# Kernel optimization log

Measured on AMD Instinct MI355X. Metric: run time of the kernel, lower is better.

## Reference

```python
import jax, jax.numpy as jnp
import numpy as np

N, T, D, H = 256, 128, 512, 1024

def setup_inputs() -> dict:
    key = jax.random.key(0)
    k = jax.random.split(key, 5)
    x = jax.random.normal(k[0], (N, T, D), dtype=jnp.float32)
    A = jax.random.normal(k[1], (N, H, 4, 4), dtype=jnp.float32)
    Wx = jax.random.normal(k[2], (D, 4 * H), dtype=jnp.float32) / np.sqrt(D)
    Wh = jax.random.normal(k[3], (H, 4 * H), dtype=jnp.float32) / np.sqrt(H)
    Wattn = jax.random.normal(k[4], (H, 4 * H), dtype=jnp.float32) / np.sqrt(H)
    b = jnp.zeros((4 * H,), dtype=jnp.float32)
    return {"x": x, "A": A, "Wx": Wx, "Wh": Wh, "Wattn": Wattn, "b": b}

def reference(x, A, Wx, Wh, Wattn, b):
    n, h_dim = A.shape[0], A.shape[1]
    A_flat = A.reshape(n, h_dim, -1)            # (N, H, L), L = 16 spatial locations
    h0 = A_flat.mean(axis=-1)                   # avg-pooled image feature
    c0 = h0
    scale = 1.0 / jnp.sqrt(jnp.asarray(h_dim, dtype=x.dtype))

    def step(carry, x_t):
        h, c = carry
        # scaled dot-product attention over the 4x4 feature grid
        scores = jnp.einsum('nhl,nh->nl', A_flat, h) * scale
        w = jax.nn.softmax(scores, axis=1)
        attn = jnp.einsum('nhl,nl->nh', A_flat, w)
        gates = x_t @ Wx + h @ Wh + attn @ Wattn + b  # (N, 4H)
        i, f, o, g = jnp.split(gates, 4, axis=1)
        c_next = jax.nn.sigmoid(f) * c + jax.nn.sigmoid(i) * jnp.tanh(g)
        h_next = jax.nn.sigmoid(o) * jnp.tanh(c_next)
        return (h_next, c_next), h_next

    (_, _), hs = jax.lax.scan(step, (h0, c0), jnp.swapaxes(x, 0, 1))
    return jnp.swapaxes(hs, 0, 1)               # (N, T, H)
```

## Files before the change

### kernel.cpp

```cpp
#include <hip/hip_runtime.h>

#define Nn 256
#define Tt 128
#define Dd 512
#define Hh 1024
#define G4 4096
#define KK 2560
#define KHALF 1280

typedef __attribute__((ext_vector_type(8))) short s8v;
typedef __attribute__((ext_vector_type(4))) float f4v;

__device__ __forceinline__ float bf2f(ushort u) {
    union { unsigned int i; float f; } v; v.i = ((unsigned int)u) << 16; return v.f;
}
__device__ __forceinline__ ushort f2bf(float f) {
    union { float f; unsigned int i; } v; v.f = f;
    unsigned int x = v.i;
    return (ushort)((x + 0x7fffu + ((x >> 16) & 1u)) >> 16);
}
__device__ __forceinline__ void split2(float f, ushort& hi, ushort& lo) {
    hi = f2bf(f);
    lo = f2bf(f - bf2f(hi));
}

__global__ __launch_bounds__(256) void prep_W(
    const float* __restrict__ Wx, const float* __restrict__ Wh,
    const float* __restrict__ Wa, ushort* __restrict__ Whi,
    ushort* __restrict__ Wlo)
{
    __shared__ float tile[64 * 65];
    int kb = blockIdx.x * 64;
    int jb = blockIdx.y * 64;
    const float* src; int kofs;
    if (kb < Dd)            { src = Wx; kofs = kb; }
    else if (kb < Dd + Hh)  { src = Wh; kofs = kb - Dd; }
    else                    { src = Wa; kofs = kb - Dd - Hh; }
    int tid = threadIdx.x;
    int r = tid >> 2;
    int c16 = (tid & 3) * 16;
    const float* sp = src + (size_t)(kofs + r) * G4 + jb + c16;
    #pragma unroll
    for (int i = 0; i < 16; i++) tile[(c16 + i) * 65 + r] = sp[i];
    __syncthreads();
    ushort hi[16], lo[16];
    #pragma unroll
    for (int i = 0; i < 16; i++) split2(tile[r * 65 + c16 + i], hi[i], lo[i]);
    size_t o = (size_t)(jb + r) * KK + kb + c16;
    #pragma unroll
    for (int p = 0; p < 2; p++) {
        s8v vh, vl;
        #pragma unroll
        for (int i = 0; i < 8; i++) { vh[i] = (short)hi[p * 8 + i]; vl[i] = (short)lo[p * 8 + i]; }
        *(s8v*)&Whi[o + p * 8] = vh;
        *(s8v*)&Wlo[o + p * 8] = vl;
    }
}

__global__ __launch_bounds__(256) void init_h0(
    const float* __restrict__ A, float* __restrict__ h, float* __restrict__ c,
    ushort* __restrict__ hhi, ushort* __restrict__ hlo)
{
    int i = blockIdx.x * 256 + threadIdx.x;
    const float* ap = A + (size_t)i * 16;
    float s = 0.f;
    #pragma unroll
    for (int l = 0; l < 16; l++) s += ap[l];
    s *= (1.f / 16.f);
    h[i] = s; c[i] = s;
    ushort hi, lo; split2(s, hi, lo);
    hhi[i] = hi; hlo[i] = lo;
}

__global__ __launch_bounds__(256) void attn_step(
    const float* __restrict__ A, const float* __restrict__ h,
    ushort* __restrict__ athi, ushort* __restrict__ atlo)
{
    int n = blockIdx.x;
    int tid = threadIdx.x;
    int lane = tid & 63, wave = tid >> 6;
    __shared__ float red[4][16];
    __shared__ float wsm[16];
    const float* An = A + (size_t)n * Hh * 16;
    float areg[4][16];
    float hreg[4];
    #pragma unroll
    for (int rr = 0; rr < 4; rr++) {
        int hh = tid + rr * 256;
        const f4v* ap = (const f4v*)(An + (size_t)hh * 16);
        #pragma unroll
        for (int q = 0; q < 4; q++) {
            f4v v = ap[q];
            areg[rr][q * 4 + 0] = v[0]; areg[rr][q * 4 + 1] = v[1];
            areg[rr][q * 4 + 2] = v[2]; areg[rr][q * 4 + 3] = v[3];
        }
        hreg[rr] = h[n * Hh + hh];
    }
    float part[16];
    #pragma unroll
    for (int l = 0; l < 16; l++) part[l] = 0.f;
    #pragma unroll
    for (int rr = 0; rr < 4; rr++)
        #pragma unroll
        for (int l = 0; l < 16; l++) part[l] += areg[rr][l] * hreg[rr];
    #pragma unroll
    for (int l = 0; l < 16; l++) {
        float v = part[l];
        #pragma unroll
        for (int off = 32; off > 0; off >>= 1) v += __shfl_down(v, off);
        if (lane == 0) red[wave][l] = v;
    }
    __syncthreads();
    if (tid == 0) {
        float sc[16]; float mx = -3.4e38f;
        #pragma unroll
        for (int l = 0; l < 16; l++) {
            sc[l] = (red[0][l] + red[1][l] + red[2][l] + red[3][l]) * 0.03125f;
            mx = fmaxf(mx, sc[l]);
        }
        float sum = 0.f;
        #pragma unroll
        for (int l = 0; l < 16; l++) { sc[l] = expf(sc[l] - mx); sum += sc[l]; }
        float inv = 1.f / sum;
        #pragma unroll
        for (int l = 0; l < 16; l++) wsm[l] = sc[l] * inv;
    }
    __syncthreads();
    float w[16];
    #pragma unroll
    for (int l = 0; l < 16; l++) w[l] = wsm[l];
    #pragma unroll
    for (int rr = 0; rr < 4; rr++) {
        int hh = tid + rr * 256;
        float s = 0.f;
        #pragma unroll
        for (int l = 0; l < 16; l++) s += areg[rr][l] * w[l];
        ushort hi, lo; split2(s, hi, lo);
        athi[n * Hh + hh] = hi; atlo[n * Hh + hh] = lo;
    }
}

__global__ __launch_bounds__(256) void gemm_half(
    const float* __restrict__ x,
    const ushort* __restrict__ hhi, const ushort* __restrict__ hlo,
    const ushort* __restrict__ athi, const ushort* __restrict__ atlo,
    const ushort* __restrict__ Whi, const ushort* __restrict__ Wlo,
    float* __restrict__ g0, float* __restrict__ g1, int t)
{
    __shared__ ushort Ahi[64 * 72], Alo[64 * 72];
    __shared__ ushort Bhi[64 * 72], Blo[64 * 72];
    int j0 = blockIdx.x * 64;
    int n0 = blockIdx.y * 64;
    int kb0 = blockIdx.z * KHALF;
    float* gout = blockIdx.z ? g1 : g0;
    int tid = threadIdx.x;
    int lane = tid & 63, wave = tid >> 6;
    int l15 = lane & 15, quad = lane >> 4;
    f4v acc[4];
    #pragma unroll
    for (int s = 0; s < 4; s++) acc[s] = (f4v){0.f, 0.f, 0.f, 0.f};

    int rs = tid >> 3;
    int cs = (tid & 7) * 8;

    for (int kb = kb0; kb < kb0 + KHALF; kb += 64) {
        __syncthreads();
        if (kb < Dd) {
            const float* xs = x + (size_t)t * Dd + kb + cs;
            #pragma unroll
            for (int p = 0; p < 2; p++) {
                int r = rs + 32 * p;
                const float* ap = xs + (size_t)(n0 + r) * (Tt * Dd);
                s8v vh, vl;
                #pragma unroll
                for (int i = 0; i < 8; i++) {
                    ushort hi_, lo_; split2(ap[i], hi_, lo_);
                    vh[i] = (short)hi_; vl[i] = (short)lo_;
                }
                *(s8v*)&Ahi[r * 72 + cs] = vh;
                *(s8v*)&Alo[r * 72 + cs] = vl;
            }
        } else {
            const ushort *sh, *sl; int kofs;
            if (kb < Dd + Hh) { sh = hhi; sl = hlo; kofs = kb - Dd; }
            else              { sh = athi; sl = atlo; kofs = kb - Dd - Hh; }
            #pragma unroll
            for (int p = 0; p < 2; p++) {
                int r = rs + 32 * p;
                size_t o = (size_t)(n0 + r) * Hh + kofs + cs;
                *(s8v*)&Ahi[r * 72 + cs] = *(const s8v*)&sh[o];
                *(s8v*)&Alo[r * 72 + cs] = *(const s8v*)&sl[o];
            }
        }
        #pragma unroll
        for (int p = 0; p < 2; p++) {
            int r = rs + 32 * p;
            size_t o = (size_t)(j0 + r) * KK + kb + cs;
            *(s8v*)&Bhi[r * 72 + cs] = *(const s8v*)&Whi[o];
            *(s8v*)&Blo[r * 72 + cs] = *(const s8v*)&Wlo[o];
        }
        __syncthreads();
        #pragma unroll
        for (int ks = 0; ks < 2; ks++) {
            s8v ah = *(const s8v*)&Ahi[(wave * 16 + l15) * 72 + ks * 32 + quad * 8];
            s8v al = *(const s8v*)&Alo[(wave * 16 + l15) * 72 + ks * 32 + quad * 8];
            #pragma unroll
            for (int s = 0; s < 4; s++) {
                s8v bh = *(const s8v*)&Bhi[(s * 16 + l15) * 72 + ks * 32 + quad * 8];
                s8v bl = *(const s8v*)&Blo[(s * 16 + l15) * 72 + ks * 32 + quad * 8];
                acc[s] = __builtin_amdgcn_mfma_f32_16x16x32_bf16(ah, bh, acc[s], 0, 0, 0);
                acc[s] = __builtin_amdgcn_mfma_f32_16x16x32_bf16(ah, bl, acc[s], 0, 0, 0);
                acc[s] = __builtin_amdgcn_mfma_f32_16x16x32_bf16(al, bh, acc[s], 0, 0, 0);
            }
        }
    }
    #pragma unroll
    for (int s = 0; s < 4; s++) {
        int j = j0 + s * 16 + l15;
        #pragma unroll
        for (int rr = 0; rr < 4; rr++) {
            int row = n0 + wave * 16 + quad * 4 + rr;
            gout[(size_t)row * G4 + j] = acc[s][rr];
        }
    }
}

__global__ __launch_bounds__(256) void lstm_update(
    const float* __restrict__ g0, const float* __restrict__ g1,
    const float* __restrict__ bias,
    float* __restrict__ c, float* __restrict__ h,
    ushort* __restrict__ hhi, ushort* __restrict__ hlo,
    float* __restrict__ out, int t)
{
    int i = blockIdx.x * 256 + threadIdx.x;
    int n = i >> 10, j = i & 1023;
    size_t base = (size_t)n * G4;
    float gi = g0[base + j]          + g1[base + j]          + bias[j];
    float gf = g0[base + Hh + j]     + g1[base + Hh + j]     + bias[Hh + j];
    float go = g0[base + 2 * Hh + j] + g1[base + 2 * Hh + j] + bias[2 * Hh + j];
    float gg = g0[base + 3 * Hh + j] + g1[base + 3 * Hh + j] + bias[3 * Hh + j];
    float si = 1.f / (1.f + expf(-gi));
    float sf = 1.f / (1.f + expf(-gf));
    float so = 1.f / (1.f + expf(-go));
    float tg = tanhf(gg);
    float cn = sf * c[i] + si * tg;
    float hn = so * tanhf(cn);
    c[i] = cn; h[i] = hn;
    ushort hi, lo; split2(hn, hi, lo);
    hhi[i] = hi; hlo[i] = lo;
    out[((size_t)n * Tt + t) * Hh + j] = hn;
}

extern "C" void kernel_launch(void* const* d_in, const int* in_sizes, int n_in,
                              void* d_out, int out_size, void* d_ws, size_t ws_size,
                              hipStream_t stream)
{
    const float* x  = (const float*)d_in[0];
    const float* A  = (const float*)d_in[1];
    const float* Wx = (const float*)d_in[2];
    const float* Wh = (const float*)d_in[3];
    const float* Wa = (const float*)d_in[4];
    const float* b  = (const float*)d_in[5];
    float* out = (float*)d_out;

    char* p = (char*)d_ws;
    ushort* Whi  = (ushort*)p;  p += (size_t)G4 * KK * 2;
    ushort* Wlo  = (ushort*)p;  p += (size_t)G4 * KK * 2;
    float*  h    = (float*)p;   p += (size_t)Nn * Hh * 4;
    float*  c    = (float*)p;   p += (size_t)Nn * Hh * 4;
    float*  g0   = (float*)p;   p += (size_t)Nn * G4 * 4;
    float*  g1   = (float*)p;   p += (size_t)Nn * G4 * 4;
    ushort* hhi  = (ushort*)p;  p += (size_t)Nn * Hh * 2;
    ushort* hlo  = (ushort*)p;  p += (size_t)Nn * Hh * 2;
    ushort* athi = (ushort*)p;  p += (size_t)Nn * Hh * 2;
    ushort* atlo = (ushort*)p;  p += (size_t)Nn * Hh * 2;

    prep_W<<<dim3(KK / 64, G4 / 64), 256, 0, stream>>>(Wx, Wh, Wa, Whi, Wlo);
    init_h0<<<(Nn * Hh) / 256, 256, 0, stream>>>(A, h, c, hhi, hlo);
    for (int t = 0; t < Tt; t++) {
        attn_step<<<Nn, 256, 0, stream>>>(A, h, athi, atlo);
        gemm_half<<<dim3(G4 / 64, Nn / 64, 2), 256, 0, stream>>>(
            x, hhi, hlo, athi, atlo, Whi, Wlo, g0, g1, t);
        lstm_update<<<(Nn * Hh) / 256, 256, 0, stream>>>(
            g0, g1, b, c, h, hhi, hlo, out, t);
    }
}
```

Measured before the change: 6.335 ms.

## Precompute A·Wattn once and fuse attention weights into LSTM update

Uses associativity: attn@Wattn = sum_l w_l (A_l@Wattn), so A@Wattn is computed once per batch row (N*16 x 4H) before the loop. The per-step GEMM K shrinks from 2560 to 1536 (x and h only), and the gate update kernel adds the weighted sum over the 16 precomputed rows. Softmax weights for the next step are computed inside the fused LSTM kernel, removing the separate attention launch. In exchange it adds a 64MB AW buffer read every step, which brings extra memory traffic.

```diff
diff --git a/kernel.cpp b/kernel.cpp
--- a/kernel.cpp
+++ b/kernel.cpp
@@ -6,9 +6,11 @@
 #define Hh 1024
 #define G4 4096
 #define KK 2560
-#define KHALF 1280
+#define KSTEP 1536
+#define KHALF 768
 
 typedef __attribute__((ext_vector_type(8))) short s8v;
+typedef __attribute__((ext_vector_type(4))) short s4v;
 typedef __attribute__((ext_vector_type(4))) float f4v;
 
 __device__ __forceinline__ float bf2f(ushort u) {
@@ -57,6 +59,93 @@
     }
 }
 
+__global__ __launch_bounds__(256) void prep_A(
+    const float* __restrict__ A, ushort* __restrict__ Athi,
+    ushort* __restrict__ Atlo)
+{
+    int n = blockIdx.x;
+    int tid = threadIdx.x;
+    int h0 = tid * 4;
+    float v[4][16];
+    #pragma unroll
+    for (int r = 0; r < 4; r++) {
+        const f4v* p = (const f4v*)(A + ((size_t)n * Hh + h0 + r) * 16);
+        #pragma unroll
+        for (int q = 0; q < 4; q++) {
+            f4v xv = p[q];
+            v[r][q * 4 + 0] = xv[0]; v[r][q * 4 + 1] = xv[1];
+            v[r][q * 4 + 2] = xv[2]; v[r][q * 4 + 3] = xv[3];
+        }
+    }
+    #pragma unroll
+    for (int l = 0; l < 16; l++) {
+        s4v vh, vl;
+        #pragma unroll
+        for (int r = 0; r < 4; r++) {
+            ushort hi, lo; split2(v[r][l], hi, lo);
+            vh[r] = (short)hi; vl[r] = (short)lo;
+        }
+        size_t o = ((size_t)n * 16 + l) * Hh + h0;
+        *(s4v*)&Athi[o] = vh;
+        *(s4v*)&Atlo[o] = vl;
+    }
+}
+
+__global__ __launch_bounds__(256) void aw_gemm(
+    const ushort* __restrict__ Athi, const ushort* __restrict__ Atlo,
+    const ushort* __restrict__ Whi, const ushort* __restrict__ Wlo,
+    float* __restrict__ AW)
+{
+    __shared__ ushort Ahi[64 * 72], Alo[64 * 72];
+    __shared__ ushort Bhi[64 * 72], Blo[64 * 72];
+    int j0 = blockIdx.x * 64;
+    int m0 = blockIdx.y * 64;
+    int tid = threadIdx.x;
+    int lane = tid & 63, wave = tid >> 6;
+    int l15 = lane & 15, quad = lane >> 4;
+    f4v acc[4];
+    #pragma unroll
+    for (int s = 0; s < 4; s++) acc[s] = (f4v){0.f, 0.f, 0.f, 0.f};
+    int rs = tid >> 3;
+    int cs = (tid & 7) * 8;
+    for (int kb = 0; kb < Hh; kb += 64) {
+        __syncthreads();
+        #pragma unroll
+        for (int p = 0; p < 2; p++) {
+            int r = rs + 32 * p;
+            size_t oa = (size_t)(m0 + r) * Hh + kb + cs;
+            *(s8v*)&Ahi[r * 72 + cs] = *(const s8v*)&Athi[oa];
+            *(s8v*)&Alo[r * 72 + cs] = *(const s8v*)&Atlo[oa];
+            size_t ob = (size_t)(j0 + r) * KK + (Dd + Hh) + kb + cs;
+            *(s8v*)&Bhi[r * 72 + cs] = *(const s8v*)&Whi[ob];
+            *(s8v*)&Blo[r * 72 + cs] = *(const s8v*)&Wlo[ob];
+        }
+        __syncthreads();
+        #pragma unroll
+        for (int ks = 0; ks < 2; ks++) {
+            s8v ah = *(const s8v*)&Ahi[(wave * 16 + l15) * 72 + ks * 32 + quad * 8];
+            s8v al = *(const s8v*)&Alo[(wave * 16 + l15) * 72 + ks * 32 + quad * 8];
+            #pragma unroll
+            for (int s = 0; s < 4; s++) {
+                s8v bh = *(const s8v*)&Bhi[(s * 16 + l15) * 72 + ks * 32 + quad * 8];
+                s8v bl = *(const s8v*)&Blo[(s * 16 + l15) * 72 + ks * 32 + quad * 8];
+                acc[s] = __builtin_amdgcn_mfma_f32_16x16x32_bf16(ah, bh, acc[s], 0, 0, 0);
+                acc[s] = __builtin_amdgcn_mfma_f32_16x16x32_bf16(ah, bl, acc[s], 0, 0, 0);
+                acc[s] = __builtin_amdgcn_mfma_f32_16x16x32_bf16(al, bh, acc[s], 0, 0, 0);
+            }
+        }
+    }
+    #pragma unroll
+    for (int s = 0; s < 4; s++) {
+        int j = j0 + s * 16 + l15;
+        #pragma unroll
+        for (int rr = 0; rr < 4; rr++) {
+            int row = m0 + wave * 16 + quad * 4 + rr;
+            AW[(size_t)row * G4 + j] = acc[s][rr];
+        }
+    }
+}
+
 __global__ __launch_bounds__(256) void init_h0(
     const float* __restrict__ A, float* __restrict__ h, float* __restrict__ c,
     ushort* __restrict__ hhi, ushort* __restrict__ hlo)
@@ -72,37 +161,29 @@
     hhi[i] = hi; hlo[i] = lo;
 }
 
-__global__ __launch_bounds__(256) void attn_step(
+__global__ __launch_bounds__(256) void calc_w(
     const float* __restrict__ A, const float* __restrict__ h,
-    ushort* __restrict__ athi, ushort* __restrict__ atlo)
+    float* __restrict__ wbuf)
 {
     int n = blockIdx.x;
     int tid = threadIdx.x;
     int lane = tid & 63, wave = tid >> 6;
     __shared__ float red[4][16];
-    __shared__ float wsm[16];
-    const float* An = A + (size_t)n * Hh * 16;
-    float areg[4][16];
-    float hreg[4];
+    float part[16];
+    #pragma unroll
+    for (int l = 0; l < 16; l++) part[l] = 0.f;
     #pragma unroll
     for (int rr = 0; rr < 4; rr++) {
         int hh = tid + rr * 256;
-        const f4v* ap = (const f4v*)(An + (size_t)hh * 16);
+        float hv = h[n * Hh + hh];
+        const f4v* ap = (const f4v*)(A + ((size_t)n * Hh + hh) * 16);
         #pragma unroll
         for (int q = 0; q < 4; q++) {
             f4v v = ap[q];
-            areg[rr][q * 4 + 0] = v[0]; areg[rr][q * 4 + 1] = v[1];
-            areg[rr][q * 4 + 2] = v[2]; areg[rr][q * 4 + 3] = v[3];
-        }
-        hreg[rr] = h[n * Hh + hh];
-    }
-    float part[16];
-    #pragma unroll
-    for (int l = 0; l < 16; l++) part[l] = 0.f;
-    #pragma unroll
-    for (int rr = 0; rr < 4; rr++)
-        #pragma unroll
-        for (int l = 0; l < 16; l++) part[l] += areg[rr][l] * hreg[rr];
+            part[q * 4 + 0] += v[0] * hv; part[q * 4 + 1] += v[1] * hv;
+            part[q * 4 + 2] += v[2] * hv; part[q * 4 + 3] += v[3] * hv;
+        }
+    }
     #pragma unroll
     for (int l = 0; l < 16; l++) {
         float v = part[l];
@@ -123,27 +204,13 @@
         for (int l = 0; l < 16; l++) { sc[l] = expf(sc[l] - mx); sum += sc[l]; }
         float inv = 1.f / sum;
         #pragma unroll
-        for (int l = 0; l < 16; l++) wsm[l] = sc[l] * inv;
-    }
-    __syncthreads();
-    float w[16];
-    #pragma unroll
-    for (int l = 0; l < 16; l++) w[l] = wsm[l];
-    #pragma unroll
-    for (int rr = 0; rr < 4; rr++) {
-        int hh = tid + rr * 256;
-        float s = 0.f;
-        #pragma unroll
-        for (int l = 0; l < 16; l++) s += areg[rr][l] * w[l];
-        ushort hi, lo; split2(s, hi, lo);
-        athi[n * Hh + hh] = hi; atlo[n * Hh + hh] = lo;
+        for (int l = 0; l < 16; l++) wbuf[n * 16 + l] = sc[l] * inv;
     }
 }
 
 __global__ __launch_bounds__(256) void gemm_half(
     const float* __restrict__ x,
     const ushort* __restrict__ hhi, const ushort* __restrict__ hlo,
-    const ushort* __restrict__ athi, const ushort* __restrict__ atlo,
     const ushort* __restrict__ Whi, const ushort* __restrict__ Wlo,
     float* __restrict__ g0, float* __restrict__ g1, int t)
 {
@@ -181,15 +248,13 @@
                 *(s8v*)&Alo[r * 72 + cs] = vl;
             }
         } else {
-            const ushort *sh, *sl; int kofs;
-            if (kb < Dd + Hh) { sh = hhi; sl = hlo; kofs = kb - Dd; }
-            else              { sh = athi; sl = atlo; kofs = kb - Dd - Hh; }
+            int kofs = kb - Dd;
             #pragma unroll
             for (int p = 0; p < 2; p++) {
                 int r = rs + 32 * p;
                 size_t o = (size_t)(n0 + r) * Hh + kofs + cs;
-                *(s8v*)&Ahi[r * 72 + cs] = *(const s8v*)&sh[o];
-                *(s8v*)&Alo[r * 72 + cs] = *(const s8v*)&sl[o];
+                *(s8v*)&Ahi[r * 72 + cs] = *(const s8v*)&hhi[o];
+                *(s8v*)&Alo[r * 72 + cs] = *(const s8v*)&hlo[o];
             }
         }
         #pragma unroll
@@ -225,30 +290,110 @@
     }
 }
 
-__global__ __launch_bounds__(256) void lstm_update(
+__global__ __launch_bounds__(256) void lstm_fused(
     const float* __restrict__ g0, const float* __restrict__ g1,
-    const float* __restrict__ bias,
-    float* __restrict__ c, float* __restrict__ h,
-    ushort* __restrict__ hhi, ushort* __restrict__ hlo,
+    const float* __restrict__ bias, const float* __restrict__ AW,
+    float* __restrict__ wbuf, const float* __restrict__ A,
+    float* __restrict__ c, ushort* __restrict__ hhi, ushort* __restrict__ hlo,
     float* __restrict__ out, int t)
 {
-    int i = blockIdx.x * 256 + threadIdx.x;
-    int n = i >> 10, j = i & 1023;
+    int n = blockIdx.x;
+    int tid = threadIdx.x;
+    int lane = tid & 63, wave = tid >> 6;
+    int j4 = tid * 4;
+    __shared__ float wsh[16];
+    __shared__ float red[4][16];
+    if (tid < 16) wsh[tid] = wbuf[n * 16 + tid];
+    __syncthreads();
+    float w[16];
+    #pragma unroll
+    for (int l = 0; l < 16; l++) w[l] = wsh[l];
+
+    f4v acc[4];
+    #pragma unroll
+    for (int q = 0; q < 4; q++) acc[q] = (f4v){0.f, 0.f, 0.f, 0.f};
+    const float* awp = AW + (size_t)n * 16 * G4;
+    #pragma unroll
+    for (int l = 0; l < 16; l++) {
+        float wl = w[l];
+        #pragma unroll
+        for (int q = 0; q < 4; q++) {
+            f4v v = *(const f4v*)&awp[(size_t)l * G4 + q * Hh + j4];
+            acc[q][0] += wl * v[0]; acc[q][1] += wl * v[1];
+            acc[q][2] += wl * v[2]; acc[q][3] += wl * v[3];
+        }
+    }
+
     size_t base = (size_t)n * G4;
-    float gi = g0[base + j]          + g1[base + j]          + bias[j];
-    float gf = g0[base + Hh + j]     + g1[base + Hh + j]     + bias[Hh + j];
-    float go = g0[base + 2 * Hh + j] + g1[base + 2 * Hh + j] + bias[2 * Hh + j];
-    float gg = g0[base + 3 * Hh + j] + g1[base + 3 * Hh + j] + bias[3 * Hh + j];
-    float si = 1.f / (1.f + expf(-gi));
-    float sf = 1.f / (1.f + expf(-gf));
-    float so = 1.f / (1.f + expf(-go));
-    float tg = tanhf(gg);
-    float cn = sf * c[i] + si * tg;
-    float hn = so * tanhf(cn);
-    c[i] = cn; h[i] = hn;
-    ushort hi, lo; split2(hn, hi, lo);
-    hhi[i] = hi; hlo[i] = lo;
-    out[((size_t)n * Tt + t) * Hh + j] = hn;
+    f4v gv[4];
+    #pragma unroll
+    for (int q = 0; q < 4; q++) {
+        f4v a0 = *(const f4v*)&g0[base + q * Hh + j4];
+        f4v a1 = *(const f4v*)&g1[base + q * Hh + j4];
+        f4v bv = *(const f4v*)&bias[q * Hh + j4];
+        #pragma unroll
+        for (int e = 0; e < 4; e++) gv[q][e] = a0[e] + a1[e] + bv[e] + acc[q][e];
+    }
+    int i4 = n * Hh + j4;
+    f4v cold = *(const f4v*)&c[i4];
+    f4v cnew, hnew;
+    #pragma unroll
+    for (int e = 0; e < 4; e++) {
+        float si = 1.f / (1.f + expf(-gv[0][e]));
+        float sf = 1.f / (1.f + expf(-gv[1][e]));
+        float so = 1.f / (1.f + expf(-gv[2][e]));
+        float tg = tanhf(gv[3][e]);
+        float cn = sf * cold[e] + si * tg;
+        float hn = so * tanhf(cn);
+        cnew[e] = cn; hnew[e] = hn;
+    }
+    *(f4v*)&c[i4] = cnew;
+    s4v vh, vl;
+    #pragma unroll
+    for (int e = 0; e < 4; e++) {
+        ushort hi, lo; split2(hnew[e], hi, lo);
+        vh[e] = (short)hi; vl[e] = (short)lo;
+    }
+    *(s4v*)&hhi[i4] = vh;
+    *(s4v*)&hlo[i4] = vl;
+    *(f4v*)&out[((size_t)n * Tt + t) * Hh + j4] = hnew;
+
+    float part[16];
+    #pragma unroll
+    for (int l = 0; l < 16; l++) part[l] = 0.f;
+    #pragma unroll
+    for (int r = 0; r < 4; r++) {
+        float hv = hnew[r];
+        const f4v* ap = (const f4v*)(A + ((size_t)n * Hh + j4 + r) * 16);
+        #pragma unroll
+        for (int q = 0; q < 4; q++) {
+            f4v v = ap[q];
+            part[q * 4 + 0] += v[0] * hv; part[q * 4 + 1] += v[1] * hv;
+            part[q * 4 + 2] += v[2] * hv; part[q * 4 + 3] += v[3] * hv;
+        }
+    }
+    #pragma unroll
+    for (int l = 0; l < 16; l++) {
+        float v = part[l];
+        #pragma unroll
+        for (int off = 32; off > 0; off >>= 1) v += __shfl_down(v, off);
+        if (lane == 0) red[wave][l] = v;
+    }
+    __syncthreads();
+    if (tid == 0) {
+        float sc[16]; float mx = -3.4e38f;
+        #pragma unroll
+        for (int l = 0; l < 16; l++) {
+            sc[l] = (red[0][l] + red[1][l] + red[2][l] + red[3][l]) * 0.03125f;
+            mx = fmaxf(mx, sc[l]);
+        }
+        float sum = 0.f;
+        #pragma unroll
+        for (int l = 0; l < 16; l++) { sc[l] = expf(sc[l] - mx); sum += sc[l]; }
+        float inv = 1.f / sum;
+        #pragma unroll
+        for (int l = 0; l < 16; l++) wbuf[n * 16 + l] = sc[l] * inv;
+    }
 }
 
 extern "C" void kernel_launch(void* const* d_in, const int* in_sizes, int n_in,
@@ -272,16 +417,21 @@
     float*  g1   = (float*)p;   p += (size_t)Nn * G4 * 4;
     ushort* hhi  = (ushort*)p;  p += (size_t)Nn * Hh * 2;
     ushort* hlo  = (ushort*)p;  p += (size_t)Nn * Hh * 2;
-    ushort* athi = (ushort*)p;  p += (size_t)Nn * Hh * 2;
-    ushort* atlo = (ushort*)p;  p += (size_t)Nn * Hh * 2;
+    ushort* Athi = (ushort*)p;  p += (size_t)Nn * 16 * Hh * 2;
+    ushort* Atlo = (ushort*)p;  p += (size_t)Nn * 16 * Hh * 2;
+    float*  AW   = (float*)p;   p += (size_t)Nn * 16 * G4 * 4;
+    float*  wbuf = (float*)p;   p += (size_t)Nn * 16 * 4;
 
     prep_W<<<dim3(KK / 64, G4 / 64), 256, 0, stream>>>(Wx, Wh, Wa, Whi, Wlo);
+    prep_A<<<Nn, 256, 0, stream>>>(A, Athi, Atlo);
+    aw_gemm<<<dim3(G4 / 64, (Nn * 16) / 64), 256, 0, stream>>>(
+        Athi, Atlo, Whi, Wlo, AW);
     init_h0<<<(Nn * Hh) / 256, 256, 0, stream>>>(A, h, c, hhi, hlo);
+    calc_w<<<Nn, 256, 0, stream>>>(A, h, wbuf);
     for (int t = 0; t < Tt; t++) {
-        attn_step<<<Nn, 256, 0, stream>>>(A, h, athi, atlo);
         gemm_half<<<dim3(G4 / 64, Nn / 64, 2), 256, 0, stream>>>(
-            x, hhi, hlo, athi, atlo, Whi, Wlo, g0, g1, t);
-        lstm_update<<<(Nn * Hh) / 256, 256, 0, stream>>>(
-            g0, g1, b, c, h, hhi, hlo, out, t);
-    }
-}
+            x, hhi, hlo, Whi, Wlo, g0, g1, t);
+        lstm_fused<<<Nn, 256, 0, stream>>>(
+            g0, g1, b, AW, wbuf, A, c, hhi, hlo, out, t);
+    }
+}
```

New measurement: 5.936 ms. 1.07x faster.
